# Kernel optimization log

Hardware: AMD Instinct MI355X
Metric: run time of the kernel (lower is better)

Reference implementation:

```python
import jax, jax.numpy as jnp
import numpy as np

B, S, H = 4, 4096, 256
NH, W = 8, 128
DH = H // NH
FF = 1024
NEG = -1e9

def gelu(x):
    return jax.nn.gelu(x, approximate=False)

def layer_norm(x, g, b, eps=1e-9):
    # torch .std() is unbiased (ddof=1); note the (std + eps) denominator, not sqrt(var+eps)
    mean = jnp.mean(x, axis=-1, keepdims=True)
    std = jnp.std(x, axis=-1, keepdims=True, ddof=1)
    return g * (x - mean) / (std + eps) + b

def causal_conv(x, w, b, dilation):
    # x: (B,S,C), w: (9, Cin, Cout); left-padded causal conv (Conv class)
    pad = dilation * 8
    y = jax.lax.conv_general_dilated(x, w, window_strides=(1,), padding=[(pad, 0)],
                                     rhs_dilation=(dilation,), dimension_numbers=('NWC', 'WIO', 'NWC'))
    return y + b

def sliding_window_attention(q, k, v, bias):
    # q,k,v: (B,NH,S,DH); q pre-scaled. Faithful to Longformer sliding_chunks_matmul_qk/pv:
    # band of 2W+1 relative offsets per query, out-of-range keys masked to -inf before softmax.
    b, h, s, d = q.shape
    c = s // W  # number of length-W query chunks
    qc = q.reshape(b, h, c, W, d)
    kp = jnp.pad(k, ((0, 0), (0, 0), (W, W), (0, 0)))
    vp = jnp.pad(v, ((0, 0), (0, 0), (W, W), (0, 0)))
    kidx = (jnp.arange(c) * W)[:, None] + jnp.arange(3 * W)[None, :]  # (c,3W) overlapping key chunks
    kc = kp[:, :, kidx, :]  # (b,h,c,3W,d)
    vc = vp[:, :, kidx, :]
    scores = jnp.einsum('bhcxd,bhcyd->bhcxy', qc, kc)  # (b,h,c,W,3W)
    x = jnp.arange(W)
    r = jnp.arange(2 * W + 1)
    band_idx = x[:, None] + r[None, :]  # (W,2W+1), values in [0,3W-1]
    band = jnp.take_along_axis(scores, band_idx[None, None, None], axis=-1)  # (b,h,c,W,2W+1)
    i = jnp.arange(s).reshape(c, W)
    j = i[:, :, None] + (r - W)[None, None, :]  # global key index per band entry
    valid = (j >= 0) & (j < s)
    band = jnp.where(valid[None, None], band + bias, NEG)  # relative bias depends only on offset
    probs = jax.nn.softmax(band.astype(jnp.float32), axis=-1).astype(q.dtype)
    ridx = jnp.arange(3 * W)[None, :] - x[:, None]  # (W,3W) inverse band->chunk map
    vmask = ((ridx >= 0) & (ridx <= 2 * W)).astype(probs.dtype)
    pc = jnp.take_along_axis(probs, jnp.clip(ridx, 0, 2 * W)[None, None, None], axis=-1) * vmask[None, None, None]
    return jnp.einsum('bhcxy,bhcyd->bhcxd', pc, vc).reshape(b, h, s, d)


def setup_inputs() -> dict:
    key = jax.random.key(0)
    ks = jax.random.split(key, 12)
    inputs = jax.random.normal(ks[0], (B, S, H), jnp.float32)
    dw_w = jax.random.normal(ks[1], (9,), jnp.float32) * 0.1   # depthwise (9,1) kernel, 1 channel
    dw_b = jnp.zeros((1,), jnp.float32)
    pw_w = jax.random.normal(ks[2], (3,), jnp.float32) * 0.5   # pointwise 1->3 conv (scalars)
    pw_b = jnp.zeros((3,), jnp.float32)
    Wq = jax.random.normal(ks[3], (H, H), jnp.float32) * 0.02
    Wk = jax.random.normal(ks[4], (H, H), jnp.float32) * 0.02
    Wv = jax.random.normal(ks[5], (H, H), jnp.float32) * 0.02
    Wo = jax.random.normal(ks[6], (H, H), jnp.float32) * 0.02
    rel_bias = jax.random.normal(ks[7], (2 * S,), jnp.float32) * 0.02
    ln1_g = jnp.ones((H,), jnp.float32); ln1_b = jnp.zeros((H,), jnp.float32)
    ln2_g = jnp.ones((H,), jnp.float32); ln2_b = jnp.zeros((H,), jnp.float32)
    w1 = jax.random.normal(ks[8], (9, H, FF), jnp.float32) * 0.02
    b1 = jnp.zeros((FF,), jnp.float32)
    w2 = jax.random.normal(ks[9], (9, FF, H), jnp.float32) * 0.02
    b2 = jnp.zeros((H,), jnp.float32)
    return {"inputs": inputs, "dw_w": dw_w, "dw_b": dw_b, "pw_w": pw_w, "pw_b": pw_b,
            "Wq": Wq, "Wk": Wk, "Wv": Wv, "Wo": Wo, "rel_bias": rel_bias,
            "ln1_g": ln1_g, "ln1_b": ln1_b, "ln2_g": ln2_g, "ln2_b": ln2_b,
            "w1": w1, "b1": b1, "w2": w2, "b2": b2}


def reference(inputs, dw_w, dw_b, pw_w, pw_b, Wq, Wk, Wv, Wo, rel_bias,
              ln1_g, ln1_b, ln2_g, ln2_b, w1, b1, w2, b2):
    x = inputs
    xn = layer_norm(x, ln1_g, ln1_b)
    # SepConv2d QKV generator: depthwise (9,1) conv along seq (shared over features), GELU,
    # pointwise 1x1 conv 1->3 channels, then GELU again (self.relu in MHA.forward)
    xp = jnp.pad(xn, ((0, 0), (4, 4), (0, 0)))
    dw = jnp.zeros_like(xn)
    for t in range(9):
        dw = dw + dw_w[t] * xp[:, t:t + S, :]
    dw = dw + dw_b[0]
    hmid = gelu(dw)
    qkv = gelu(hmid[None] * pw_w.reshape(3, 1, 1, 1) + pw_b.reshape(3, 1, 1, 1))  # (3,B,S,H)
    q = qkv[0] @ Wq
    k = qkv[1] @ Wk
    v = qkv[2] @ Wv
    split = lambda t: t.reshape(B, S, NH, DH).transpose(0, 2, 1, 3)
    q, k, v = split(q), split(k), split(v)
    q = q * (DH ** -0.5)
    # relative_position_index = arange(2W+1).repeat(lens,1) -> bias uses table[:2W+1] per offset
    bias = rel_bias[:2 * W + 1]
    ctx = sliding_window_attention(q, k, v, bias)
    ctx = ctx.transpose(0, 2, 1, 3).reshape(B, S, H)
    x = x + ctx @ Wo
    xn2 = layer_norm(x, ln2_g, ln2_b)
    # PositionwiseFeedForward 'cc': causal dilated convs; GELU applied after every layer (incl. last)
    f = gelu(causal_conv(xn2, w1, b1, 1))
    f = gelu(causal_conv(f, w2, b2, 8))
    return x + f
```

## Files before the change

### kernel.cpp

```cpp
#include <hip/hip_runtime.h>
#include <stdint.h>

typedef uint16_t u16;
typedef uint32_t u32;

typedef __attribute__((ext_vector_type(8))) short bf16x8;
typedef __attribute__((ext_vector_type(4))) float f32x4;

typedef __attribute__((address_space(1))) const u32 gas_u32;
typedef __attribute__((address_space(3))) u32 las_u32;

#define S_LEN 4096
#define HDIM  256
#define FFDIM 1024

__device__ __forceinline__ float bf2f(u16 u) { return __uint_as_float(((u32)u) << 16); }
__device__ __forceinline__ u16 f2bf(float f) {
  u32 x = __float_as_uint(f);
  return (u16)((x + 0x7fffu + ((x >> 16) & 1u)) >> 16);
}
__device__ __forceinline__ float gelu_f(float x) {
  return 0.5f * x * (1.0f + erff(x * 0.7071067811865475f));
}
__device__ __forceinline__ void glds16(const u16* g, u16* l) {
  __builtin_amdgcn_global_load_lds((gas_u32*)g, (las_u32*)l, 16, 0, 0);
}

__global__ __launch_bounds__(256) void zero_guards(uint4* __restrict__ xn2p, uint4* __restrict__ f1p) {
  int t = blockIdx.x * 256 + threadIdx.x;
  const uint4 z = {0u, 0u, 0u, 0u};
  if (t < 1024) {
    const int s = t >> 8, o = t & 255;
    xn2p[(long)s * 131328 + o] = z;
  } else {
    t -= 1024;
    if (t < 32768) {
      const int s = t >> 13, o = t & 8191;
      f1p[(long)s * 532480 + o] = z;
    }
  }
}

__global__ __launch_bounds__(256) void ktranspose(const float* __restrict__ in, u16* __restrict__ out,
                                                  int K, int N, float scale) {
  __shared__ u16 t[32][33];
  const int k0 = blockIdx.x * 32, n0 = blockIdx.y * 32;
  const int tx = threadIdx.x, ty = threadIdx.y;
#pragma unroll
  for (int i = ty; i < 32; i += 8) t[i][tx] = f2bf(in[(long)(k0 + i) * N + (n0 + tx)] * scale);
  __syncthreads();
#pragma unroll
  for (int i = ty; i < 32; i += 8) out[(long)(n0 + i) * K + (k0 + tx)] = t[tx][i];
}

template <int OUTBF>
__global__ __launch_bounds__(256) void ln_kernel(const float* __restrict__ inv, void* __restrict__ outv,
                                                 const float* __restrict__ g, const float* __restrict__ bsh,
                                                 int OSEGR, int OGUARD) {
  const int tid = threadIdx.x;
  const int lane = tid & 63;
  const long row = (long)blockIdx.x * 4 + (tid >> 6);
  const int c0 = lane * 4;
  float v[4];
  float4 f = *(const float4*)(inv + row * HDIM + c0);
  v[0] = f.x; v[1] = f.y; v[2] = f.z; v[3] = f.w;
  float s = v[0] + v[1] + v[2] + v[3];
#pragma unroll
  for (int o = 32; o > 0; o >>= 1) s += __shfl_xor(s, o);
  const float mean = s * (1.0f / 256.0f);
  float ss = 0.f;
#pragma unroll
  for (int j = 0; j < 4; ++j) { float d = v[j] - mean; ss += d * d; }
#pragma unroll
  for (int o = 32; o > 0; o >>= 1) ss += __shfl_xor(ss, o);
  const float inv_ = 1.0f / (sqrtf(ss * (1.0f / 255.0f)) + 1e-9f);
  float y[4];
#pragma unroll
  for (int j = 0; j < 4; ++j) y[j] = g[c0 + j] * (v[j] - mean) * inv_ + bsh[c0 + j];
  if (OUTBF) {
    const long orow = (row >> 12) * OSEGR + OGUARD + (row & (S_LEN - 1));
    uint2 o_;
    o_.x = (u32)f2bf(y[0]) | ((u32)f2bf(y[1]) << 16);
    o_.y = (u32)f2bf(y[2]) | ((u32)f2bf(y[3]) << 16);
    *(uint2*)((u16*)outv + orow * HDIM + c0) = o_;
  } else {
    float4 o_; o_.x = y[0]; o_.y = y[1]; o_.z = y[2]; o_.w = y[3];
    *(float4*)((float*)outv + row * HDIM + c0) = o_;
  }
}

__global__ __launch_bounds__(256) void dwconv_qkv(const float* __restrict__ xn,
                                                  u16* __restrict__ gq, u16* __restrict__ gk, u16* __restrict__ gv,
                                                  const float* __restrict__ dw_w, const float* __restrict__ dw_b,
                                                  const float* __restrict__ pw_w, const float* __restrict__ pw_b) {
  const int tid = threadIdx.x;
  const int lane = tid & 63;
  const long row = (long)blockIdx.x * 4 + (tid >> 6);
  const int sl = (int)(row & (S_LEN - 1));
  const float b0 = dw_b[0];
  float a0 = b0, a1 = b0, a2 = b0, a3 = b0;
#pragma unroll
  for (int t = 0; t < 9; ++t) {
    const int s2 = sl + t - 4;
    if (s2 >= 0 && s2 < S_LEN) {
      const float w = dw_w[t];
      float4 xv = *(const float4*)(xn + (row + t - 4) * HDIM + lane * 4);
      a0 = fmaf(w, xv.x, a0); a1 = fmaf(w, xv.y, a1);
      a2 = fmaf(w, xv.z, a2); a3 = fmaf(w, xv.w, a3);
    }
  }
  float h[4];
  h[0] = gelu_f(a0); h[1] = gelu_f(a1); h[2] = gelu_f(a2); h[3] = gelu_f(a3);
  u16* outs[3] = {gq, gk, gv};
#pragma unroll
  for (int p = 0; p < 3; ++p) {
    const float pw = pw_w[p], pb = pw_b[p];
    float y[4];
#pragma unroll
    for (int j = 0; j < 4; ++j) y[j] = gelu_f(fmaf(h[j], pw, pb));
    uint2 o_;
    o_.x = (u32)f2bf(y[0]) | ((u32)f2bf(y[1]) << 16);
    o_.y = (u32)f2bf(y[2]) | ((u32)f2bf(y[3]) << 16);
    *(uint2*)(outs[p] + row * HDIM + lane * 4) = o_;
  }
}

template <int EPI>
__global__ __launch_bounds__(256) void gemm_glds(
    const u16* __restrict__ A, const u16* __restrict__ BT, void* __restrict__ Outv,
    u16* __restrict__ vt, const float* __restrict__ residv, int KW, int N,
    long a_z, long b_z, long o_z) {
  __shared__ __align__(16) u16 As[128 * 64];
  __shared__ __align__(16) u16 Bs[128 * 64];
  const int tid = threadIdx.x;
  const int lane = tid & 63;
  const int wid = tid >> 6;
  const int wm = (wid & 1) * 64;
  const int wn = (wid >> 1) * 64;
  const int fm = lane & 15;
  const int fq = lane >> 4;
  const int t0 = blockIdx.x * 128;
  const int n0 = blockIdx.y * 128;
  A += (long)blockIdx.z * a_z;
  BT += (long)blockIdx.z * b_z;

  const int srow = lane >> 3;
  const int cseg = (((lane & 7) ^ srow) << 3);

  f32x4 acc[4][4];
#pragma unroll
  for (int a = 0; a < 4; ++a)
#pragma unroll
    for (int b = 0; b < 4; ++b) acc[a][b] = (f32x4){0.f, 0.f, 0.f, 0.f};

  u16* alb = &As[wid * 32 * 64];
  u16* blb = &Bs[wid * 32 * 64];

  for (int k0 = 0; k0 < KW; k0 += 64) {
    const u16* ag = A + (long)(t0 + wid * 32 + srow) * KW + k0 + cseg;
    const u16* bg = BT + (long)(n0 + wid * 32 + srow) * KW + k0 + cseg;
#pragma unroll
    for (int j = 0; j < 4; ++j) {
      glds16(ag + (long)(8 * j) * KW, alb + j * 8 * 64);
      glds16(bg + (long)(8 * j) * KW, blb + j * 8 * 64);
    }
    __syncthreads();
#pragma unroll
    for (int kk = 0; kk < 2; ++kk) {
      const int g = kk * 4 + fq;
      bf16x8 af[4], bfv[4];
#pragma unroll
      for (int t = 0; t < 4; ++t) {
        const int ra = wm + t * 16 + fm;
        af[t] = *(const bf16x8*)&As[ra * 64 + ((g ^ (ra & 7)) << 3)];
        const int rb = wn + t * 16 + fm;
        bfv[t] = *(const bf16x8*)&Bs[rb * 64 + ((g ^ (rb & 7)) << 3)];
      }
#pragma unroll
      for (int mi = 0; mi < 4; ++mi)
#pragma unroll
        for (int ni = 0; ni < 4; ++ni)
          acc[mi][ni] = __builtin_amdgcn_mfma_f32_16x16x32_bf16(af[mi], bfv[ni], acc[mi][ni], 0, 0, 0);
    }
    __syncthreads();
  }

#pragma unroll
  for (int mi = 0; mi < 4; ++mi)
#pragma unroll
    for (int ni = 0; ni < 4; ++ni) {
      if (EPI == 0 && blockIdx.z == 2) {
        const int col = n0 + wn + ni * 16 + fm;
        const int hh = col >> 5, dd = col & 31;
        const long trow0 = t0 + wm + mi * 16 + fq * 4;
        const long bb = trow0 >> 12;
        const int s0 = (int)(trow0 & (S_LEN - 1));
        uint2 o_;
        o_.x = (u32)f2bf(acc[mi][ni][0]) | ((u32)f2bf(acc[mi][ni][1]) << 16);
        o_.y = (u32)f2bf(acc[mi][ni][2]) | ((u32)f2bf(acc[mi][ni][3]) << 16);
        *(uint2*)(vt + ((bb * 8 + hh) * 32 + dd) * S_LEN + s0) = o_;
      } else {
#pragma unroll
        for (int r = 0; r < 4; ++r) {
          const long trow = t0 + wm + mi * 16 + fq * 4 + r;
          const int col = n0 + wn + ni * 16 + fm;
          const float cv = acc[mi][ni][r];
          if (EPI == 0) {
            ((u16*)Outv + (long)blockIdx.z * o_z)[trow * N + col] = f2bf(cv);
          } else {
            ((float*)Outv)[trow * N + col] = cv + residv[trow * N + col];
          }
        }
      }
    }
}

__global__ __launch_bounds__(256) void attn_mfma(const u16* __restrict__ Q, const u16* __restrict__ K,
                                                 const u16* __restrict__ VT, const float* __restrict__ rel,
                                                 u16* __restrict__ CTX) {
  __shared__ __align__(16) u16 Ks[384 * 36];
  __shared__ __align__(16) u16 VTs[32 * 388];
  __shared__ __align__(16) u16 Ps[4][32 * 72];
  __shared__ float bias_s[260];
  const int c = blockIdx.x, h = blockIdx.y, b = blockIdx.z;
  const int tid = threadIdx.x;
  const int lane = tid & 63, wid = tid >> 6;
  const int fm = lane & 15, fq = lane >> 4;
  const int j0 = c * 128 - 128;
  const long kvbase = ((long)b * S_LEN) * HDIM + h * 32;
  const long vtbase = (((long)b * 8 + h) * 32) * S_LEN;

  for (int idx = tid; idx < 384 * 4; idx += 256) {
    const int jj = idx >> 2, seg = (idx & 3) * 8;
    int j = j0 + jj; j = j < 0 ? 0 : (j > S_LEN - 1 ? S_LEN - 1 : j);
    uint4 kv = *(const uint4*)(K + kvbase + (long)j * HDIM + seg);
    *(uint4*)&Ks[jj * 36 + seg] = kv;
  }
#pragma unroll
  for (int p = 0; p < 6; ++p) {
    const int idx = p * 256 + tid;
    const int d = idx / 48, seg = idx - d * 48;
    int off = j0 + seg * 8; off = off < 0 ? 0 : (off > S_LEN - 8 ? S_LEN - 8 : off);
    uint4 vv = *(const uint4*)(VT + vtbase + (long)d * S_LEN + off);
    *(uint4*)&VTs[d * 388 + seg * 8] = vv;
  }
  for (int idx = tid; idx < 257; idx += 256) bias_s[idx] = rel[idx];
  __syncthreads();

  bf16x8 aq[2];
#pragma unroll
  for (int mi = 0; mi < 2; ++mi)
    aq[mi] = *(const bf16x8*)(Q + kvbase + (long)(c * 128 + wid * 32 + mi * 16 + fm) * HDIM + fq * 8);

  const int klo = (c == 0) ? 128 : 0;
  const int khi = (c == 31) ? 255 : 383;

  float m_r[2][4], l_r[2][4];
  f32x4 acc[2][2];
#pragma unroll
  for (int mi = 0; mi < 2; ++mi)
#pragma unroll
    for (int r = 0; r < 4; ++r) { m_r[mi][r] = -1e9f; l_r[mi][r] = 0.f; }
#pragma unroll
  for (int mi = 0; mi < 2; ++mi)
#pragma unroll
    for (int nd = 0; nd < 2; ++nd) acc[mi][nd] = (f32x4){0.f, 0.f, 0.f, 0.f};

  u16* pw = &Ps[wid][0];

  for (int ch = 0; ch < 6; ++ch) {
    f32x4 sc[2][4];
#pragma unroll
    for (int ni = 0; ni < 4; ++ni) {
      bf16x8 bk = *(const bf16x8*)&Ks[(ch * 64 + ni * 16 + fm) * 36 + fq * 8];
#pragma unroll
      for (int mi = 0; mi < 2; ++mi)
        sc[mi][ni] = __builtin_amdgcn_mfma_f32_16x16x32_bf16(aq[mi], bk, (f32x4){0.f, 0.f, 0.f, 0.f}, 0, 0, 0);
    }
    float cm[2][4];
#pragma unroll
    for (int mi = 0; mi < 2; ++mi)
#pragma unroll
      for (int r = 0; r < 4; ++r) cm[mi][r] = -1e9f;
#pragma unroll
    for (int mi = 0; mi < 2; ++mi)
#pragma unroll
      for (int ni = 0; ni < 4; ++ni) {
        const int keyloc = ch * 64 + ni * 16 + fm;
        const bool kval = (keyloc >= klo) && (keyloc <= khi);
#pragma unroll
        for (int r = 0; r < 4; ++r) {
          const int qloc = wid * 32 + mi * 16 + fq * 4 + r;
          const int rr = keyloc - qloc;
          const bool valid = kval && (rr >= 0) && (rr <= 256);
          const int rc = valid ? rr : 0;
          float vv = sc[mi][ni][r] + bias_s[rc];
          vv = valid ? vv : -1e9f;
          sc[mi][ni][r] = vv;
          cm[mi][r] = fmaxf(cm[mi][r], vv);
        }
      }
#pragma unroll
    for (int mi = 0; mi < 2; ++mi)
#pragma unroll
      for (int r = 0; r < 4; ++r) {
        float x = cm[mi][r];
        x = fmaxf(x, __shfl_xor(x, 1));
        x = fmaxf(x, __shfl_xor(x, 2));
        x = fmaxf(x, __shfl_xor(x, 4));
        x = fmaxf(x, __shfl_xor(x, 8));
        cm[mi][r] = x;
      }
    float alpha[2][4];
#pragma unroll
    for (int mi = 0; mi < 2; ++mi)
#pragma unroll
      for (int r = 0; r < 4; ++r) {
        const float nm = fmaxf(m_r[mi][r], cm[mi][r]);
        alpha[mi][r] = __expf(m_r[mi][r] - nm);
        m_r[mi][r] = nm;
        l_r[mi][r] *= alpha[mi][r];
      }
#pragma unroll
    for (int mi = 0; mi < 2; ++mi)
#pragma unroll
      for (int nd = 0; nd < 2; ++nd)
#pragma unroll
        for (int r = 0; r < 4; ++r) acc[mi][nd][r] *= alpha[mi][r];
#pragma unroll
    for (int mi = 0; mi < 2; ++mi)
#pragma unroll
      for (int ni = 0; ni < 4; ++ni)
#pragma unroll
        for (int r = 0; r < 4; ++r) {
          const float pv = __expf(sc[mi][ni][r] - m_r[mi][r]);
          l_r[mi][r] += pv;
          pw[(mi * 16 + fq * 4 + r) * 72 + ni * 16 + fm] = f2bf(pv);
        }
#pragma unroll
    for (int kc = 0; kc < 2; ++kc) {
      bf16x8 ap[2], bv[2];
#pragma unroll
      for (int mi = 0; mi < 2; ++mi)
        ap[mi] = *(const bf16x8*)&pw[(mi * 16 + fm) * 72 + kc * 32 + fq * 8];
#pragma unroll
      for (int nd = 0; nd < 2; ++nd)
        bv[nd] = *(const bf16x8*)&VTs[(nd * 16 + fm) * 388 + ch * 64 + kc * 32 + fq * 8];
#pragma unroll
      for (int mi = 0; mi < 2; ++mi)
#pragma unroll
        for (int nd = 0; nd < 2; ++nd)
          acc[mi][nd] = __builtin_amdgcn_mfma_f32_16x16x32_bf16(ap[mi], bv[nd], acc[mi][nd], 0, 0, 0);
    }
  }

  float linv[2][4];
#pragma unroll
  for (int mi = 0; mi < 2; ++mi)
#pragma unroll
    for (int r = 0; r < 4; ++r) {
      float x = l_r[mi][r];
      x += __shfl_xor(x, 1);
      x += __shfl_xor(x, 2);
      x += __shfl_xor(x, 4);
      x += __shfl_xor(x, 8);
      linv[mi][r] = 1.0f / x;
    }
#pragma unroll
  for (int mi = 0; mi < 2; ++mi)
#pragma unroll
    for (int nd = 0; nd < 2; ++nd)
#pragma unroll
      for (int r = 0; r < 4; ++r) {
        const long s = c * 128 + wid * 32 + mi * 16 + fq * 4 + r;
        CTX[((long)b * S_LEN + s) * HDIM + h * 32 + nd * 16 + fm] = f2bf(acc[mi][nd][r] * linv[mi][r]);
      }
}

template <int EPI>
__global__ __launch_bounds__(256) void gemm_conv(
    const u16* __restrict__ Apad, const u16* __restrict__ BT, void* __restrict__ Outv,
    const float* __restrict__ bias,
    int APITCH, int SEGR, int BPITCH, int ntaps, int dil,
    int N, int OSEGR, int OGUARD, long out_z_off) {
  __shared__ __align__(16) u16 As[144 * 64];
  __shared__ __align__(16) u16 Bs2[2][128 * 64];
  const int tid = threadIdx.x;
  const int lane = tid & 63;
  const int wid = tid >> 6;
  const int wm = (wid & 1) * 64;
  const int wn = (wid >> 1) * 64;
  const int fm = lane & 15;
  const int fq = lane >> 4;
  const int t0 = blockIdx.x * 128;
  const int n0 = blockIdx.y * 128;
  const int tap0 = blockIdx.z * ntaps;

  const int seg = t0 >> 12;
  const long abase = (long)seg * SEGR + (t0 & (S_LEN - 1)) + (long)tap0 * dil;
  const int aops = (128 + (ntaps - 1) * dil + 7) >> 3;

  const int srow = lane >> 3;
  const int cseg = (((lane & 7) ^ srow) << 3);

  f32x4 acc[4][4];
#pragma unroll
  for (int a = 0; a < 4; ++a)
#pragma unroll
    for (int b = 0; b < 4; ++b) acc[a][b] = (f32x4){0.f, 0.f, 0.f, 0.f};

  for (int k0 = 0; k0 < APITCH; k0 += 64) {
    for (int op = wid; op < aops; op += 4)
      glds16(Apad + (abase + op * 8 + srow) * APITCH + k0 + cseg, &As[op * 8 * 64]);
    {
      const long bc = (long)tap0 * APITCH + k0;
#pragma unroll
      for (int j = 0; j < 4; ++j)
        glds16(BT + (long)(n0 + wid * 32 + j * 8 + srow) * BPITCH + bc + cseg,
               &Bs2[0][(wid * 32 + j * 8) * 64]);
    }
    __syncthreads();
    for (int u = 0; u < ntaps; ++u) {
      if (u + 1 < ntaps) {
        const long bc = (long)(tap0 + u + 1) * APITCH + k0;
#pragma unroll
        for (int j = 0; j < 4; ++j)
          glds16(BT + (long)(n0 + wid * 32 + j * 8 + srow) * BPITCH + bc + cseg,
                 &Bs2[(u + 1) & 1][(wid * 32 + j * 8) * 64]);
      }
      const int du = u * dil;
      const u16* bsp = Bs2[u & 1];
#pragma unroll
      for (int kk = 0; kk < 2; ++kk) {
        const int g = kk * 4 + fq;
        bf16x8 af[4], bfv[4];
#pragma unroll
        for (int t = 0; t < 4; ++t) {
          const int ra = wm + t * 16 + fm + du;
          af[t] = *(const bf16x8*)&As[ra * 64 + ((g ^ (ra & 7)) << 3)];
          const int rb = wn + t * 16 + fm;
          bfv[t] = *(const bf16x8*)&bsp[rb * 64 + ((g ^ (rb & 7)) << 3)];
        }
#pragma unroll
        for (int mi = 0; mi < 4; ++mi)
#pragma unroll
          for (int ni = 0; ni < 4; ++ni)
            acc[mi][ni] = __builtin_amdgcn_mfma_f32_16x16x32_bf16(af[mi], bfv[ni], acc[mi][ni], 0, 0, 0);
      }
      __syncthreads();
    }
  }

#pragma unroll
  for (int mi = 0; mi < 4; ++mi)
#pragma unroll
    for (int ni = 0; ni < 4; ++ni)
#pragma unroll
      for (int r = 0; r < 4; ++r) {
        const long trow = t0 + wm + mi * 16 + fq * 4 + r;
        const int col = n0 + wn + ni * 16 + fm;
        const float cv = acc[mi][ni][r];
        if (EPI == 2) {
          const long orow = (trow >> 12) * OSEGR + OGUARD + (trow & (S_LEN - 1));
          ((u16*)Outv)[orow * N + col] = f2bf(gelu_f(cv + bias[col]));
        } else {
          (((float*)Outv) + (long)blockIdx.z * out_z_off)[trow * N + col] = cv;
        }
      }
}

__global__ __launch_bounds__(256) void final_kernel(const float* __restrict__ x2, const float* __restrict__ P,
                                                    const float* __restrict__ b2, float* __restrict__ out) {
  const long i4 = ((long)blockIdx.x * 256 + threadIdx.x) * 4;
  const int c0 = (int)(i4 & (HDIM - 1));
  float4 xa = *(const float4*)(x2 + i4);
  float4 p0 = *(const float4*)(P + i4);
  float4 p1 = *(const float4*)(P + 4194304 + i4);
  float4 p2 = *(const float4*)(P + 8388608 + i4);
  const float pv[4] = {p0.x + p1.x + p2.x, p0.y + p1.y + p2.y, p0.z + p1.z + p2.z, p0.w + p1.w + p2.w};
  float4 o_;
  o_.x = xa.x + gelu_f(pv[0] + b2[c0 + 0]);
  o_.y = xa.y + gelu_f(pv[1] + b2[c0 + 1]);
  o_.z = xa.z + gelu_f(pv[2] + b2[c0 + 2]);
  o_.w = xa.w + gelu_f(pv[3] + b2[c0 + 3]);
  *(float4*)(out + i4) = o_;
}

extern "C" void kernel_launch(void* const* d_in, const int* in_sizes, int n_in,
                              void* d_out, int out_size, void* d_ws, size_t ws_size,
                              hipStream_t stream) {
  (void)in_sizes; (void)n_in; (void)out_size;
  const float* X    = (const float*)d_in[0];
  const float* dw_w = (const float*)d_in[1];
  const float* dw_b = (const float*)d_in[2];
  const float* pw_w = (const float*)d_in[3];
  const float* pw_b = (const float*)d_in[4];
  const float* Wq   = (const float*)d_in[5];
  const float* Wk   = (const float*)d_in[6];
  const float* Wv   = (const float*)d_in[7];
  const float* Wo   = (const float*)d_in[8];
  const float* rel  = (const float*)d_in[9];
  const float* ln1g = (const float*)d_in[10];
  const float* ln1b = (const float*)d_in[11];
  const float* ln2g = (const float*)d_in[12];
  const float* ln2b = (const float*)d_in[13];
  const float* w1   = (const float*)d_in[14];
  const float* b1   = (const float*)d_in[15];
  const float* w2   = (const float*)d_in[16];
  const float* b2   = (const float*)d_in[17];

  if (ws_size < 119537664) return;

  char* ws = (char*)d_ws;
  u16* WqT = (u16*)(ws + 0);
  u16* WkT = (u16*)(ws + 131072);
  u16* WvT = (u16*)(ws + 262144);
  u16* WoT = (u16*)(ws + 393216);
  u16* W1T = (u16*)(ws + 524288);
  u16* W2T = (u16*)(ws + 5242880);
  float* xn  = (float*)(ws + 10485760);
  float* x2  = xn;
  u16* gq  = (u16*)(ws + 27262976);
  u16* gk  = (u16*)(ws + 35651584);
  u16* gv  = (u16*)(ws + 44040192);
  u16* q   = (u16*)(ws + 52428800);
  u16* vt  = (u16*)(ws + 69206016);
  u16* ctx = (u16*)(ws + 77594624);
  u16* f1p  = (u16*)(ws + 27262976);
  u16* xn2p = (u16*)(ws + 61341696);
  float* P  = (float*)(ws + 61341696);

  const float qscale = 0.17677669529663687f;
  dim3 tb(32, 8);
  ktranspose<<<dim3(8, 8), tb, 0, stream>>>(Wq, WqT, 256, 256, qscale);
  ktranspose<<<dim3(8, 8), tb, 0, stream>>>(Wk, WkT, 256, 256, 1.0f);
  ktranspose<<<dim3(8, 8), tb, 0, stream>>>(Wv, WvT, 256, 256, 1.0f);
  ktranspose<<<dim3(8, 8), tb, 0, stream>>>(Wo, WoT, 256, 256, 1.0f);
  ktranspose<<<dim3(72, 32), tb, 0, stream>>>(w1, W1T, 2304, 1024, 1.0f);
  ktranspose<<<dim3(288, 8), tb, 0, stream>>>(w2, W2T, 9216, 256, 1.0f);

  ln_kernel<0><<<4096, 256, 0, stream>>>(X, xn, ln1g, ln1b, 4096, 0);
  dwconv_qkv<<<4096, 256, 0, stream>>>(xn, gq, gk, gv, dw_w, dw_b, pw_w, pw_b);

  gemm_glds<0><<<dim3(128, 2, 3), 256, 0, stream>>>(gq, WqT, q, vt, nullptr,
      256, 256, 4194304, 65536, 4194304);

  attn_mfma<<<dim3(32, 8, 4), 256, 0, stream>>>(q, q + 4194304, vt, rel, ctx);

  gemm_glds<1><<<dim3(128, 2), 256, 0, stream>>>(ctx, WoT, x2, nullptr, X, 256, 256, 0, 0, 0);

  zero_guards<<<132, 256, 0, stream>>>((uint4*)xn2p, (uint4*)f1p);

  ln_kernel<1><<<4096, 256, 0, stream>>>(x2, xn2p, ln2g, ln2b, 4104, 8);

  gemm_conv<2><<<dim3(128, 8), 256, 0, stream>>>(xn2p, W1T, f1p, b1,
      256, 4104, 2304, 9, 1, 1024, 4160, 64, 0);

  gemm_conv<3><<<dim3(128, 2, 3), 256, 0, stream>>>(f1p, W2T, P, nullptr,
      1024, 4160, 9216, 3, 8, 256, 0, 0, 4194304);

  final_kernel<<<4096, 256, 0, stream>>>(x2, P, b2, (float*)d_out);
}
```

Measured before the change: 393.8 us.

## Enlarge conv GEMM tiles to 256 rows and split second conv over K

Both causal-conv GEMMs now use 256-row output tiles, with each wave covering 128x64, so every B tile loaded to LDS is reused across twice as many rows. The second conv previously split its 9 taps across grid z. It now splits the input-channel dimension across z, so each block runs all taps on one shared A halo tile. Shapes, taps and dilation become template constants so loops fully unroll. The cost is a larger accumulator and LDS footprint and fewer blocks in each grid, which can reduce occupancy and load balance.

```diff
diff --git a/kernel.cpp b/kernel.cpp
--- a/kernel.cpp
+++ b/kernel.cpp
@@ -377,72 +377,75 @@
       }
 }
 
-template <int EPI>
-__global__ __launch_bounds__(256) void gemm_conv(
+template <int EPI, int APITCH, int NTAPS, int DIL, int NN, int ZSPLIT>
+__global__ __launch_bounds__(256, 2) void gemm_conv(
     const u16* __restrict__ Apad, const u16* __restrict__ BT, void* __restrict__ Outv,
     const float* __restrict__ bias,
-    int APITCH, int SEGR, int BPITCH, int ntaps, int dil,
-    int N, int OSEGR, int OGUARD, long out_z_off) {
-  __shared__ __align__(16) u16 As[144 * 64];
+    int SEGR, int BPITCH, int OSEGR, int OGUARD, long out_z_off) {
+  constexpr int AROWS = 256 + (NTAPS - 1) * DIL;
+  constexpr int AOPS = (AROWS + 7) / 8;
+  constexpr int KITERS = APITCH / 64;
+  __shared__ __align__(16) u16 As[AOPS * 8 * 64];
   __shared__ __align__(16) u16 Bs2[2][128 * 64];
   const int tid = threadIdx.x;
   const int lane = tid & 63;
   const int wid = tid >> 6;
-  const int wm = (wid & 1) * 64;
+  const int wm = (wid & 1) * 128;
   const int wn = (wid >> 1) * 64;
   const int fm = lane & 15;
   const int fq = lane >> 4;
-  const int t0 = blockIdx.x * 128;
+  const int t0 = blockIdx.x * 256;
   const int n0 = blockIdx.y * 128;
-  const int tap0 = blockIdx.z * ntaps;
+  const int zz = blockIdx.z;
+  const int k_lo = ((zz * KITERS) / ZSPLIT) * 64;
+  const int k_hi = (((zz + 1) * KITERS) / ZSPLIT) * 64;
 
   const int seg = t0 >> 12;
-  const long abase = (long)seg * SEGR + (t0 & (S_LEN - 1)) + (long)tap0 * dil;
-  const int aops = (128 + (ntaps - 1) * dil + 7) >> 3;
-
+  const long abase = (long)seg * SEGR + (t0 & (S_LEN - 1));
   const int srow = lane >> 3;
   const int cseg = (((lane & 7) ^ srow) << 3);
 
-  f32x4 acc[4][4];
-#pragma unroll
-  for (int a = 0; a < 4; ++a)
+  f32x4 acc[8][4];
+#pragma unroll
+  for (int a = 0; a < 8; ++a)
 #pragma unroll
     for (int b = 0; b < 4; ++b) acc[a][b] = (f32x4){0.f, 0.f, 0.f, 0.f};
 
-  for (int k0 = 0; k0 < APITCH; k0 += 64) {
-    for (int op = wid; op < aops; op += 4)
+  for (int k0 = k_lo; k0 < k_hi; k0 += 64) {
+    for (int op = wid; op < AOPS; op += 4)
       glds16(Apad + (abase + op * 8 + srow) * APITCH + k0 + cseg, &As[op * 8 * 64]);
-    {
-      const long bc = (long)tap0 * APITCH + k0;
-#pragma unroll
-      for (int j = 0; j < 4; ++j)
-        glds16(BT + (long)(n0 + wid * 32 + j * 8 + srow) * BPITCH + bc + cseg,
-               &Bs2[0][(wid * 32 + j * 8) * 64]);
-    }
+#pragma unroll
+    for (int j = 0; j < 4; ++j)
+      glds16(BT + (long)(n0 + wid * 32 + j * 8 + srow) * BPITCH + k0 + cseg,
+             &Bs2[0][(wid * 32 + j * 8) * 64]);
     __syncthreads();
-    for (int u = 0; u < ntaps; ++u) {
-      if (u + 1 < ntaps) {
-        const long bc = (long)(tap0 + u + 1) * APITCH + k0;
+#pragma unroll
+    for (int u = 0; u < NTAPS; ++u) {
+      if (u + 1 < NTAPS) {
+        const long bc = (long)(u + 1) * APITCH + k0;
 #pragma unroll
         for (int j = 0; j < 4; ++j)
           glds16(BT + (long)(n0 + wid * 32 + j * 8 + srow) * BPITCH + bc + cseg,
                  &Bs2[(u + 1) & 1][(wid * 32 + j * 8) * 64]);
       }
-      const int du = u * dil;
+      const int du = u * DIL;
       const u16* bsp = Bs2[u & 1];
 #pragma unroll
       for (int kk = 0; kk < 2; ++kk) {
         const int g = kk * 4 + fq;
-        bf16x8 af[4], bfv[4];
-#pragma unroll
-        for (int t = 0; t < 4; ++t) {
+        bf16x8 af[8], bfv[4];
+#pragma unroll
+        for (int t = 0; t < 8; ++t) {
           const int ra = wm + t * 16 + fm + du;
           af[t] = *(const bf16x8*)&As[ra * 64 + ((g ^ (ra & 7)) << 3)];
+        }
+#pragma unroll
+        for (int t = 0; t < 4; ++t) {
           const int rb = wn + t * 16 + fm;
           bfv[t] = *(const bf16x8*)&bsp[rb * 64 + ((g ^ (rb & 7)) << 3)];
         }
 #pragma unroll
-        for (int mi = 0; mi < 4; ++mi)
+        for (int mi = 0; mi < 8; ++mi)
 #pragma unroll
           for (int ni = 0; ni < 4; ++ni)
             acc[mi][ni] = __builtin_amdgcn_mfma_f32_16x16x32_bf16(af[mi], bfv[ni], acc[mi][ni], 0, 0, 0);
@@ -452,7 +455,7 @@
   }
 
 #pragma unroll
-  for (int mi = 0; mi < 4; ++mi)
+  for (int mi = 0; mi < 8; ++mi)
 #pragma unroll
     for (int ni = 0; ni < 4; ++ni)
 #pragma unroll
@@ -462,9 +465,9 @@
         const float cv = acc[mi][ni][r];
         if (EPI == 2) {
           const long orow = (trow >> 12) * OSEGR + OGUARD + (trow & (S_LEN - 1));
-          ((u16*)Outv)[orow * N + col] = f2bf(gelu_f(cv + bias[col]));
+          ((u16*)Outv)[orow * NN + col] = f2bf(gelu_f(cv + bias[col]));
         } else {
-          (((float*)Outv) + (long)blockIdx.z * out_z_off)[trow * N + col] = cv;
+          (((float*)Outv) + (long)zz * out_z_off)[trow * NN + col] = cv;
         }
       }
 }
@@ -553,11 +556,11 @@
 
   ln_kernel<1><<<4096, 256, 0, stream>>>(x2, xn2p, ln2g, ln2b, 4104, 8);
 
-  gemm_conv<2><<<dim3(128, 8), 256, 0, stream>>>(xn2p, W1T, f1p, b1,
-      256, 4104, 2304, 9, 1, 1024, 4160, 64, 0);
-
-  gemm_conv<3><<<dim3(128, 2, 3), 256, 0, stream>>>(f1p, W2T, P, nullptr,
-      1024, 4160, 9216, 3, 8, 256, 0, 0, 4194304);
+  gemm_conv<2, 256, 9, 1, 1024, 1><<<dim3(64, 8, 1), 256, 0, stream>>>(
+      xn2p, W1T, f1p, b1, 4104, 2304, 4160, 64, 0);
+
+  gemm_conv<3, 1024, 9, 8, 256, 3><<<dim3(64, 2, 3), 256, 0, stream>>>(
+      f1p, W2T, P, nullptr, 4160, 9216, 0, 0, 4194304);
 
   final_kernel<<<4096, 256, 0, stream>>>(x2, P, b2, (float*)d_out);
 }
```

Result: slower. 408.8 us (+3.8%).

## Enlarge GEMM M-tiles to 256 rows and merge small setup kernels

Applied to the files above, without the earlier changes.

The QKV projection and the first causal-conv GEMM now use 256x128 tiles, with each wave holding 8x4 MFMA accumulators. This doubles reuse of every B-tile load and lets the conv kernel share one halo-extended A tile across all taps. The conv kernel is specialised by template on pitch, taps and dilation, and asks for two blocks per CU. The six weight-transpose launches become one kernel, and guard zeroing moves into extra blocks of the second layernorm launch, which cuts launch overhead. The larger tiles raise register and LDS pressure and halve the grid size, which may hurt occupancy.

```diff
diff --git a/kernel.cpp b/kernel.cpp
--- a/kernel.cpp
+++ b/kernel.cpp
@@ -26,25 +26,27 @@
   __builtin_amdgcn_global_load_lds((gas_u32*)g, (las_u32*)l, 16, 0, 0);
 }
 
-__global__ __launch_bounds__(256) void zero_guards(uint4* __restrict__ xn2p, uint4* __restrict__ f1p) {
-  int t = blockIdx.x * 256 + threadIdx.x;
-  const uint4 z = {0u, 0u, 0u, 0u};
-  if (t < 1024) {
-    const int s = t >> 8, o = t & 255;
-    xn2p[(long)s * 131328 + o] = z;
+__global__ __launch_bounds__(256) void ktranspose_all(
+    const float* __restrict__ Wq, const float* __restrict__ Wk, const float* __restrict__ Wv,
+    const float* __restrict__ Wo, const float* __restrict__ W1, const float* __restrict__ W2,
+    u16* __restrict__ WqT, u16* __restrict__ WkT, u16* __restrict__ WvT,
+    u16* __restrict__ WoT, u16* __restrict__ W1T, u16* __restrict__ W2T, float qscale) {
+  __shared__ u16 t[32][33];
+  const int bid = blockIdx.x;
+  const float* in; u16* out; int K, N; float scale = 1.0f; int idx;
+  if (bid < 256) {
+    K = 256; N = 256; idx = bid & 63;
+    const int w = bid >> 6;
+    in = (w == 0) ? Wq : (w == 1) ? Wk : (w == 2) ? Wv : Wo;
+    out = (w == 0) ? WqT : (w == 1) ? WkT : (w == 2) ? WvT : WoT;
+    if (w == 0) scale = qscale;
+  } else if (bid < 2560) {
+    K = 2304; N = 1024; idx = bid - 256; in = W1; out = W1T;
   } else {
-    t -= 1024;
-    if (t < 32768) {
-      const int s = t >> 13, o = t & 8191;
-      f1p[(long)s * 532480 + o] = z;
-    }
-  }
-}
-
-__global__ __launch_bounds__(256) void ktranspose(const float* __restrict__ in, u16* __restrict__ out,
-                                                  int K, int N, float scale) {
-  __shared__ u16 t[32][33];
-  const int k0 = blockIdx.x * 32, n0 = blockIdx.y * 32;
+    K = 9216; N = 256; idx = bid - 2560; in = W2; out = W2T;
+  }
+  const int kt = K >> 5;
+  const int k0 = (idx % kt) * 32, n0 = (idx / kt) * 32;
   const int tx = threadIdx.x, ty = threadIdx.y;
 #pragma unroll
   for (int i = ty; i < 32; i += 8) t[i][tx] = f2bf(in[(long)(k0 + i) * N + (n0 + tx)] * scale);
@@ -56,8 +58,24 @@
 template <int OUTBF>
 __global__ __launch_bounds__(256) void ln_kernel(const float* __restrict__ inv, void* __restrict__ outv,
                                                  const float* __restrict__ g, const float* __restrict__ bsh,
-                                                 int OSEGR, int OGUARD) {
+                                                 int OSEGR, int OGUARD,
+                                                 uint4* __restrict__ gx, uint4* __restrict__ gf) {
   const int tid = threadIdx.x;
+  if (OUTBF && blockIdx.x >= 4096) {
+    int t = (blockIdx.x - 4096) * 256 + tid;
+    const uint4 z = {0u, 0u, 0u, 0u};
+    if (t < 1024) {
+      const int s = t >> 8, o = t & 255;
+      gx[(long)s * 131328 + o] = z;
+    } else {
+      t -= 1024;
+      if (t < 32768) {
+        const int s = t >> 13, o = t & 8191;
+        gf[(long)s * 532480 + o] = z;
+      }
+    }
+    return;
+  }
   const int lane = tid & 63;
   const long row = (long)blockIdx.x * 4 + (tid >> 6);
   const int c0 = lane * 4;
@@ -125,11 +143,91 @@
   }
 }
 
-template <int EPI>
-__global__ __launch_bounds__(256) void gemm_glds(
+__global__ __launch_bounds__(256) void gemm_big(
     const u16* __restrict__ A, const u16* __restrict__ BT, void* __restrict__ Outv,
-    u16* __restrict__ vt, const float* __restrict__ residv, int KW, int N,
-    long a_z, long b_z, long o_z) {
+    u16* __restrict__ vt, int KW, int N, long a_z, long b_z, long o_z) {
+  __shared__ __align__(16) u16 As[256 * 64];
+  __shared__ __align__(16) u16 Bs[128 * 64];
+  const int tid = threadIdx.x;
+  const int lane = tid & 63;
+  const int wid = tid >> 6;
+  const int wm = (wid & 1) * 128;
+  const int wn = (wid >> 1) * 64;
+  const int fm = lane & 15;
+  const int fq = lane >> 4;
+  const int t0 = blockIdx.x * 256;
+  const int n0 = blockIdx.y * 128;
+  A += (long)blockIdx.z * a_z;
+  BT += (long)blockIdx.z * b_z;
+
+  const int srow = lane >> 3;
+  const int cseg = (((lane & 7) ^ srow) << 3);
+
+  f32x4 acc[8][4];
+#pragma unroll
+  for (int a = 0; a < 8; ++a)
+#pragma unroll
+    for (int b = 0; b < 4; ++b) acc[a][b] = (f32x4){0.f, 0.f, 0.f, 0.f};
+
+  for (int k0 = 0; k0 < KW; k0 += 64) {
+    for (int op = wid; op < 32; op += 4)
+      glds16(A + (long)(t0 + op * 8 + srow) * KW + k0 + cseg, &As[op * 8 * 64]);
+#pragma unroll
+    for (int j = 0; j < 4; ++j)
+      glds16(BT + (long)(n0 + wid * 32 + j * 8 + srow) * KW + k0 + cseg,
+             &Bs[(wid * 32 + j * 8) * 64]);
+    __syncthreads();
+#pragma unroll
+    for (int kk = 0; kk < 2; ++kk) {
+      const int g = kk * 4 + fq;
+      bf16x8 af[8], bfv[4];
+#pragma unroll
+      for (int t = 0; t < 8; ++t) {
+        const int ra = wm + t * 16 + fm;
+        af[t] = *(const bf16x8*)&As[ra * 64 + ((g ^ (ra & 7)) << 3)];
+      }
+#pragma unroll
+      for (int t = 0; t < 4; ++t) {
+        const int rb = wn + t * 16 + fm;
+        bfv[t] = *(const bf16x8*)&Bs[rb * 64 + ((g ^ (rb & 7)) << 3)];
+      }
+#pragma unroll
+      for (int mi = 0; mi < 8; ++mi)
+#pragma unroll
+        for (int ni = 0; ni < 4; ++ni)
+          acc[mi][ni] = __builtin_amdgcn_mfma_f32_16x16x32_bf16(af[mi], bfv[ni], acc[mi][ni], 0, 0, 0);
+    }
+    __syncthreads();
+  }
+
+#pragma unroll
+  for (int mi = 0; mi < 8; ++mi)
+#pragma unroll
+    for (int ni = 0; ni < 4; ++ni) {
+      if (blockIdx.z == 2) {
+        const int col = n0 + wn + ni * 16 + fm;
+        const int hh = col >> 5, dd = col & 31;
+        const long trow0 = t0 + wm + mi * 16 + fq * 4;
+        const long bb = trow0 >> 12;
+        const int s0 = (int)(trow0 & (S_LEN - 1));
+        uint2 o_;
+        o_.x = (u32)f2bf(acc[mi][ni][0]) | ((u32)f2bf(acc[mi][ni][1]) << 16);
+        o_.y = (u32)f2bf(acc[mi][ni][2]) | ((u32)f2bf(acc[mi][ni][3]) << 16);
+        *(uint2*)(vt + ((bb * 8 + hh) * 32 + dd) * S_LEN + s0) = o_;
+      } else {
+#pragma unroll
+        for (int r = 0; r < 4; ++r) {
+          const long trow = t0 + wm + mi * 16 + fq * 4 + r;
+          const int col = n0 + wn + ni * 16 + fm;
+          ((u16*)Outv + (long)blockIdx.z * o_z)[trow * N + col] = f2bf(acc[mi][ni][r]);
+        }
+      }
+    }
+}
+
+__global__ __launch_bounds__(256) void gemm_wo(
+    const u16* __restrict__ A, const u16* __restrict__ BT, float* __restrict__ Outv,
+    const float* __restrict__ residv, int KW, int N) {
   __shared__ __align__(16) u16 As[128 * 64];
   __shared__ __align__(16) u16 Bs[128 * 64];
   const int tid = threadIdx.x;
@@ -141,8 +239,6 @@
   const int fq = lane >> 4;
   const int t0 = blockIdx.x * 128;
   const int n0 = blockIdx.y * 128;
-  A += (long)blockIdx.z * a_z;
-  BT += (long)blockIdx.z * b_z;
 
   const int srow = lane >> 3;
   const int cseg = (((lane & 7) ^ srow) << 3);
@@ -188,31 +284,13 @@
 #pragma unroll
   for (int mi = 0; mi < 4; ++mi)
 #pragma unroll
-    for (int ni = 0; ni < 4; ++ni) {
-      if (EPI == 0 && blockIdx.z == 2) {
+    for (int ni = 0; ni < 4; ++ni)
+#pragma unroll
+      for (int r = 0; r < 4; ++r) {
+        const long trow = t0 + wm + mi * 16 + fq * 4 + r;
         const int col = n0 + wn + ni * 16 + fm;
-        const int hh = col >> 5, dd = col & 31;
-        const long trow0 = t0 + wm + mi * 16 + fq * 4;
-        const long bb = trow0 >> 12;
-        const int s0 = (int)(trow0 & (S_LEN - 1));
-        uint2 o_;
-        o_.x = (u32)f2bf(acc[mi][ni][0]) | ((u32)f2bf(acc[mi][ni][1]) << 16);
-        o_.y = (u32)f2bf(acc[mi][ni][2]) | ((u32)f2bf(acc[mi][ni][3]) << 16);
-        *(uint2*)(vt + ((bb * 8 + hh) * 32 + dd) * S_LEN + s0) = o_;
-      } else {
-#pragma unroll
-        for (int r = 0; r < 4; ++r) {
-          const long trow = t0 + wm + mi * 16 + fq * 4 + r;
-          const int col = n0 + wn + ni * 16 + fm;
-          const float cv = acc[mi][ni][r];
-          if (EPI == 0) {
-            ((u16*)Outv + (long)blockIdx.z * o_z)[trow * N + col] = f2bf(cv);
-          } else {
-            ((float*)Outv)[trow * N + col] = cv + residv[trow * N + col];
-          }
-        }
-      }
-    }
+        Outv[trow * N + col] = acc[mi][ni][r] + residv[trow * N + col];
+      }
 }
 
 __global__ __launch_bounds__(256) void attn_mfma(const u16* __restrict__ Q, const u16* __restrict__ K,
@@ -377,12 +455,95 @@
       }
 }
 
-template <int EPI>
-__global__ __launch_bounds__(256) void gemm_conv(
+template <int APITCH, int NTAPS, int DIL, int NN>
+__global__ __launch_bounds__(256, 2) void gemm_conv(
     const u16* __restrict__ Apad, const u16* __restrict__ BT, void* __restrict__ Outv,
     const float* __restrict__ bias,
-    int APITCH, int SEGR, int BPITCH, int ntaps, int dil,
-    int N, int OSEGR, int OGUARD, long out_z_off) {
+    int SEGR, int BPITCH, int OSEGR, int OGUARD) {
+  constexpr int AROWS = 256 + (NTAPS - 1) * DIL;
+  constexpr int AOPS = (AROWS + 7) / 8;
+  __shared__ __align__(16) u16 As[AOPS * 8 * 64];
+  __shared__ __align__(16) u16 Bs2[2][128 * 64];
+  const int tid = threadIdx.x;
+  const int lane = tid & 63;
+  const int wid = tid >> 6;
+  const int wm = (wid & 1) * 128;
+  const int wn = (wid >> 1) * 64;
+  const int fm = lane & 15;
+  const int fq = lane >> 4;
+  const int t0 = blockIdx.x * 256;
+  const int n0 = blockIdx.y * 128;
+
+  const int seg = t0 >> 12;
+  const long abase = (long)seg * SEGR + (t0 & (S_LEN - 1));
+  const int srow = lane >> 3;
+  const int cseg = (((lane & 7) ^ srow) << 3);
+
+  f32x4 acc[8][4];
+#pragma unroll
+  for (int a = 0; a < 8; ++a)
+#pragma unroll
+    for (int b = 0; b < 4; ++b) acc[a][b] = (f32x4){0.f, 0.f, 0.f, 0.f};
+
+  for (int k0 = 0; k0 < APITCH; k0 += 64) {
+    for (int op = wid; op < AOPS; op += 4)
+      glds16(Apad + (abase + op * 8 + srow) * APITCH + k0 + cseg, &As[op * 8 * 64]);
+#pragma unroll
+    for (int j = 0; j < 4; ++j)
+      glds16(BT + (long)(n0 + wid * 32 + j * 8 + srow) * BPITCH + k0 + cseg,
+             &Bs2[0][(wid * 32 + j * 8) * 64]);
+    __syncthreads();
+#pragma unroll
+    for (int u = 0; u < NTAPS; ++u) {
+      if (u + 1 < NTAPS) {
+        const long bc = (long)(u + 1) * APITCH + k0;
+#pragma unroll
+        for (int j = 0; j < 4; ++j)
+          glds16(BT + (long)(n0 + wid * 32 + j * 8 + srow) * BPITCH + bc + cseg,
+                 &Bs2[(u + 1) & 1][(wid * 32 + j * 8) * 64]);
+      }
+      const int du = u * DIL;
+      const u16* bsp = Bs2[u & 1];
+#pragma unroll
+      for (int kk = 0; kk < 2; ++kk) {
+        const int g = kk * 4 + fq;
+        bf16x8 af[8], bfv[4];
+#pragma unroll
+        for (int t = 0; t < 8; ++t) {
+          const int ra = wm + t * 16 + fm + du;
+          af[t] = *(const bf16x8*)&As[ra * 64 + ((g ^ (ra & 7)) << 3)];
+        }
+#pragma unroll
+        for (int t = 0; t < 4; ++t) {
+          const int rb = wn + t * 16 + fm;
+          bfv[t] = *(const bf16x8*)&bsp[rb * 64 + ((g ^ (rb & 7)) << 3)];
+        }
+#pragma unroll
+        for (int mi = 0; mi < 8; ++mi)
+#pragma unroll
+          for (int ni = 0; ni < 4; ++ni)
+            acc[mi][ni] = __builtin_amdgcn_mfma_f32_16x16x32_bf16(af[mi], bfv[ni], acc[mi][ni], 0, 0, 0);
+      }
+      __syncthreads();
+    }
+  }
+
+#pragma unroll
+  for (int mi = 0; mi < 8; ++mi)
+#pragma unroll
+    for (int ni = 0; ni < 4; ++ni)
+#pragma unroll
+      for (int r = 0; r < 4; ++r) {
+        const long trow = t0 + wm + mi * 16 + fq * 4 + r;
+        const int col = n0 + wn + ni * 16 + fm;
+        const long orow = (trow >> 12) * OSEGR + OGUARD + (trow & (S_LEN - 1));
+        ((u16*)Outv)[orow * NN + col] = f2bf(gelu_f(acc[mi][ni][r] + bias[col]));
+      }
+}
+
+__global__ __launch_bounds__(256) void gemm_conv_s(
+    const u16* __restrict__ Apad, const u16* __restrict__ BT, float* __restrict__ Outv,
+    int APITCH, int SEGR, int BPITCH, int ntaps, int dil, int N, long out_z_off) {
   __shared__ __align__(16) u16 As[144 * 64];
   __shared__ __align__(16) u16 Bs2[2][128 * 64];
   const int tid = threadIdx.x;
@@ -459,13 +620,7 @@
       for (int r = 0; r < 4; ++r) {
         const long trow = t0 + wm + mi * 16 + fq * 4 + r;
         const int col = n0 + wn + ni * 16 + fm;
-        const float cv = acc[mi][ni][r];
-        if (EPI == 2) {
-          const long orow = (trow >> 12) * OSEGR + OGUARD + (trow & (S_LEN - 1));
-          ((u16*)Outv)[orow * N + col] = f2bf(gelu_f(cv + bias[col]));
-        } else {
-          (((float*)Outv) + (long)blockIdx.z * out_z_off)[trow * N + col] = cv;
-        }
+        (Outv + (long)blockIdx.z * out_z_off)[trow * N + col] = acc[mi][ni][r];
       }
 }
 
@@ -531,33 +686,27 @@
   float* P  = (float*)(ws + 61341696);
 
   const float qscale = 0.17677669529663687f;
-  dim3 tb(32, 8);
-  ktranspose<<<dim3(8, 8), tb, 0, stream>>>(Wq, WqT, 256, 256, qscale);
-  ktranspose<<<dim3(8, 8), tb, 0, stream>>>(Wk, WkT, 256, 256, 1.0f);
-  ktranspose<<<dim3(8, 8), tb, 0, stream>>>(Wv, WvT, 256, 256, 1.0f);
-  ktranspose<<<dim3(8, 8), tb, 0, stream>>>(Wo, WoT, 256, 256, 1.0f);
-  ktranspose<<<dim3(72, 32), tb, 0, stream>>>(w1, W1T, 2304, 1024, 1.0f);
-  ktranspose<<<dim3(288, 8), tb, 0, stream>>>(w2, W2T, 9216, 256, 1.0f);
-
-  ln_kernel<0><<<4096, 256, 0, stream>>>(X, xn, ln1g, ln1b, 4096, 0);
+  ktranspose_all<<<4864, dim3(32, 8), 0, stream>>>(Wq, Wk, Wv, Wo, w1, w2,
+      WqT, WkT, WvT, WoT, W1T, W2T, qscale);
+
+  ln_kernel<0><<<4096, 256, 0, stream>>>(X, xn, ln1g, ln1b, 4096, 0, nullptr, nullptr);
   dwconv_qkv<<<4096, 256, 0, stream>>>(xn, gq, gk, gv, dw_w, dw_b, pw_w, pw_b);
 
-  gemm_glds<0><<<dim3(128, 2, 3), 256, 0, stream>>>(gq, WqT, q, vt, nullptr,
+  gemm_big<<<dim3(64, 2, 3), 256, 0, stream>>>(gq, WqT, q, vt,
       256, 256, 4194304, 65536, 4194304);
 
   attn_mfma<<<dim3(32, 8, 4), 256, 0, stream>>>(q, q + 4194304, vt, rel, ctx);
 
-  gemm_glds<1><<<dim3(128, 2), 256, 0, stream>>>(ctx, WoT, x2, nullptr, X, 256, 256, 0, 0, 0);
-
-  zero_guards<<<132, 256, 0, stream>>>((uint4*)xn2p, (uint4*)f1p);
-
-  ln_kernel<1><<<4096, 256, 0, stream>>>(x2, xn2p, ln2g, ln2b, 4104, 8);
-
-  gemm_conv<2><<<dim3(128, 8), 256, 0, stream>>>(xn2p, W1T, f1p, b1,
-      256, 4104, 2304, 9, 1, 1024, 4160, 64, 0);
-
-  gemm_conv<3><<<dim3(128, 2, 3), 256, 0, stream>>>(f1p, W2T, P, nullptr,
-      1024, 4160, 9216, 3, 8, 256, 0, 0, 4194304);
+  gemm_wo<<<dim3(128, 2), 256, 0, stream>>>(ctx, WoT, x2, X, 256, 256);
+
+  ln_kernel<1><<<4228, 256, 0, stream>>>(x2, xn2p, ln2g, ln2b, 4104, 8,
+      (uint4*)xn2p, (uint4*)f1p);
+
+  gemm_conv<256, 9, 1, 1024><<<dim3(64, 8), 256, 0, stream>>>(
+      xn2p, W1T, f1p, b1, 4104, 2304, 4160, 64);
+
+  gemm_conv_s<<<dim3(128, 2, 3), 256, 0, stream>>>(f1p, W2T, P,
+      1024, 4160, 9216, 3, 8, 256, 4194304);
 
   final_kernel<<<4096, 256, 0, stream>>>(x2, P, b2, (float*)d_out);
 }
```

Measured after the change: 389.2 us. About the same (-1.2%).
